# Performance work log

Measured on AMD Instinct MI355X. Metric: run time of the kernel, lower is better.

The kernel has to match this reference:

```python
import jax, jax.numpy as jnp
import numpy as np

N_NODES = 8192
N_EDGES = 49152
IN_F, HID, H1, H2, OUT_F = 128, 64, 64, 5, 32
N_BONDS = 64


def setup_inputs() -> dict:
    key = jax.random.key(0)
    ks = jax.random.split(key, 12)
    s = 0.05
    return {
        "x": jax.random.normal(ks[0], (N_NODES, IN_F), jnp.float32),
        "edge_index": jax.random.randint(ks[1], (2, N_EDGES), 0, N_NODES, jnp.int32),
        "lefts": jax.random.randint(ks[2], (N_BONDS,), 0, N_NODES, jnp.int32),
        "rights": jax.random.randint(ks[3], (N_BONDS,), 0, N_NODES, jnp.int32),
        "W1": jax.random.normal(ks[4], (H1 * HID, IN_F), jnp.float32) * s,
        "att_src1": jax.random.normal(ks[5], (H1, HID), jnp.float32) * s,
        "att_dst1": jax.random.normal(ks[6], (H1, HID), jnp.float32) * s,
        "b1": jnp.zeros((H1 * HID,), jnp.float32),
        "W2": jax.random.normal(ks[7], (H2 * OUT_F, H1 * HID), jnp.float32) * s,
        "att_src2": jax.random.normal(ks[8], (H2, OUT_F), jnp.float32) * s,
        "att_dst2": jax.random.normal(ks[9], (H2, OUT_F), jnp.float32) * s,
        "b2": jnp.zeros((OUT_F,), jnp.float32),
    }


def _gat_conv(x, src, dst, W, a_src, a_dst, b, concat):
    # x: [N, F_in]; W: [H*C, F_in]; a_src/a_dst: [H, C]
    N = x.shape[0]
    H, C = a_src.shape
    h = (x @ W.T).reshape(N, H, C)                    # [N, H, C]
    alpha_s = jnp.einsum("nhc,hc->nh", h, a_src)      # [N, H]
    alpha_d = jnp.einsum("nhc,hc->nh", h, a_dst)
    logits = jax.nn.leaky_relu(alpha_s[src] + alpha_d[dst], negative_slope=0.2)  # [E, H]
    # scatter-softmax over incoming edges of each destination node
    m = jax.ops.segment_max(logits, dst, num_segments=N)
    e = jnp.exp(logits - m[dst])
    denom = jax.ops.segment_sum(e, dst, num_segments=N)
    alpha = e / denom[dst]                            # [E, H]
    msg = h[src] * alpha[:, :, None]                  # [E, H, C]
    out = jax.ops.segment_sum(msg, dst, num_segments=N)  # [N, H, C]
    out = out.reshape(N, H * C) if concat else out.mean(axis=1)
    return out + b


def reference(x, edge_index, lefts, rights, W1, att_src1, att_dst1, b1,
              W2, att_src2, att_dst2, b2):
    N = x.shape[0]
    loops = jnp.arange(N, dtype=edge_index.dtype)
    src = jnp.concatenate([edge_index[0], loops])
    dst = jnp.concatenate([edge_index[1], loops])
    x1 = jax.nn.elu(_gat_conv(x, src, dst, W1, att_src1, att_dst1, b1, concat=True))
    x2 = _gat_conv(x1, src, dst, W2, att_src2, att_dst2, b2, concat=False)  # [N, OUT_F]
    score = (x2[lefts] + x2[rights]).sum(axis=-1)     # [N_BONDS]
    return jax.nn.softmax(score, axis=0)
```

## Files before the change

kernel.cpp:

```cpp
#include <hip/hip_runtime.h>
#include <hip/hip_bf16.h>
#include <math.h>

#define N_NODES  8192
#define N_EDGES  49152
#define E_TOT    57344
#define IN_F     128
#define HID      64
#define NH1      64
#define NH2      5
#define OUT_F    32
#define F1       4096
#define F2       160
#define N_BONDS  64
#define ET       16
#define NP       4
#define HG       16

typedef short bf16x8 __attribute__((ext_vector_type(8)));
typedef float f32x4  __attribute__((ext_vector_type(4)));

__device__ __forceinline__ float lrelu(float x){ return x > 0.f ? x : 0.2f*x; }

__device__ __forceinline__ unsigned short bf16_rne(float f){
    unsigned u = __float_as_uint(f);
    unsigned r = u + 0x7FFF + ((u >> 16) & 1);
    return (unsigned short)(r >> 16);
}
__device__ __forceinline__ float bf16f(unsigned short h){
    return __uint_as_float((unsigned)h << 16);
}

__device__ __forceinline__ void block_sync_lds(){
    asm volatile("s_waitcnt lgkmcnt(0)" ::: "memory");
    __builtin_amdgcn_s_barrier();
    asm volatile("" ::: "memory");
}

__global__ void k_init_counts(int* counts){
    int i = blockIdx.x*256 + threadIdx.x;
    if (i < N_NODES) counts[i] = 1;
}
__global__ void k_count(const int* __restrict__ ei, int* counts){
    int i = blockIdx.x*256 + threadIdx.x;
    if (i < N_EDGES) atomicAdd(&counts[ei[N_EDGES + i]], 1);
}
__global__ __launch_bounds__(1024) void k_scan(const int* __restrict__ counts,
                                               int* __restrict__ row_start,
                                               int* __restrict__ cursor){
    __shared__ int sd[1024];
    int t = threadIdx.x;
    int v[8]; int sum = 0;
    #pragma unroll
    for (int i=0;i<8;i++){ v[i] = counts[t*8+i]; sum += v[i]; }
    sd[t] = sum; __syncthreads();
    for (int off=1; off<1024; off<<=1){
        int vv = (t >= off) ? sd[t-off] : 0;
        __syncthreads();
        sd[t] += vv;
        __syncthreads();
    }
    int run = sd[t] - sum;
    #pragma unroll
    for (int i=0;i<8;i++){ row_start[t*8+i] = run; cursor[t*8+i] = run; run += v[i]; }
    if (t == 1023) row_start[N_NODES] = run;
}
__global__ void k_fill(const int* __restrict__ ei, int* cursor, int* __restrict__ csr_src){
    int i = blockIdx.x*256 + threadIdx.x;
    if (i >= E_TOT) return;
    int s, d;
    if (i < N_EDGES){ s = ei[i]; d = ei[N_EDGES + i]; }
    else { s = i - N_EDGES; d = s; }
    int pos = atomicAdd(&cursor[d], 1);
    csr_src[pos] = s;
}

__global__ void k_packw1d(const float* __restrict__ W1,
                          unsigned short* __restrict__ fh, unsigned short* __restrict__ fl){
    int g = blockIdx.x*256 + threadIdx.x;
    int lane = g & 63, ct = (g >> 6) & 3, ks = (g >> 8) & 3, hg = g >> 10;
    int col = hg*64 + ct*16 + (lane & 15);
    int k = ks*32 + (lane >> 4)*8;
    const float* src = W1 + (size_t)col*IN_F + k;
    bf16x8 hv, lv;
    #pragma unroll
    for (int j=0;j<8;j++){
        float f = src[j];
        unsigned short hb = bf16_rne(f);
        hv[j] = (short)hb;
        lv[j] = (short)bf16_rne(f - bf16f(hb));
    }
    *(bf16x8*)(fh + (size_t)g*8) = hv;
    *(bf16x8*)(fl + (size_t)g*8) = lv;
}

__global__ void k_packw2d(const float* __restrict__ W2,
                          unsigned short* __restrict__ fh, unsigned short* __restrict__ fl){
    int g = blockIdx.x*256 + threadIdx.x;
    int lane = g & 63, ni = (g >> 6) % 10, kc = g / 640;
    int n = ni*16 + (lane & 15);
    int k = kc*32 + (lane >> 4)*8;
    const float* src = W2 + (size_t)n*F1 + k;
    bf16x8 hv, lv;
    #pragma unroll
    for (int j=0;j<8;j++){
        float f = src[j];
        unsigned short hb = bf16_rne(f);
        hv[j] = (short)hb;
        lv[j] = (short)bf16_rne(f - bf16f(hb));
    }
    *(bf16x8*)(fh + (size_t)g*8) = hv;
    *(bf16x8*)(fl + (size_t)g*8) = lv;
}

__global__ __launch_bounds__(128) void k_attvec(const float* __restrict__ W1,
        const float* __restrict__ a_s, const float* __restrict__ a_d,
        float* __restrict__ vsT, float* __restrict__ vdT){
    int h = blockIdx.x, k = threadIdx.x;
    float s = 0.f, d = 0.f;
    for (int c = 0; c < HID; c++){
        float w = W1[(size_t)(h*HID + c)*IN_F + k];
        s += a_s[h*HID + c] * w;
        d += a_d[h*HID + c] * w;
    }
    vsT[k*NH1 + h] = s;
    vdT[k*NH1 + h] = d;
}

__global__ __launch_bounds__(128) void k_alpha1x(const float* __restrict__ x,
        const float* __restrict__ vsT, const float* __restrict__ vdT,
        float* __restrict__ as1, float* __restrict__ ad1){
    int n = blockIdx.x, t = threadIdx.x;
    __shared__ float xs[IN_F];
    xs[t] = x[(size_t)n*IN_F + t];
    __syncthreads();
    if (t < NH1){
        float s = 0.f, d = 0.f;
        for (int k = 0; k < IN_F; k++){
            float xv = xs[k];
            s += xv * vsT[k*NH1 + t];
            d += xv * vdT[k*NH1 + t];
        }
        as1[n*NH1 + t] = s;
        ad1[n*NH1 + t] = d;
    }
}

__global__ __launch_bounds__(256) void k_aggx64(const float* __restrict__ x,
        const float* __restrict__ as1, const float* __restrict__ ad1,
        const int* __restrict__ row_start, const int* __restrict__ csr_src,
        unsigned short* __restrict__ txhi){
    int n = blockIdx.x, t = threadIdx.x;
    __shared__ float ad_s[NH1];
    __shared__ float wt[ET][NH1];
    __shared__ int   st[ET];
    __shared__ float xs[ET][IN_F];
    int e0 = row_start[n], e1 = row_start[n+1];
    if (t < NH1) ad_s[t] = ad1[n*NH1 + t];
    int hq = t >> 4, f0 = (t & 15)*8;
    float acc[4][8] = {};
    float D[4] = {0.f, 0.f, 0.f, 0.f};
    for (int eb = e0; eb < e1; eb += ET){
        int ne = min(ET, e1 - eb);
        if (t < ne) st[t] = csr_src[eb + t];
        __syncthreads();
        for (int idx = t; idx < ne*32; idx += 256){
            int e = idx >> 5, f4 = idx & 31;
            *(float4*)&xs[e][f4*4] = *(const float4*)(x + (size_t)st[e]*IN_F + f4*4);
        }
        for (int idx = t; idx < ne*NH1; idx += 256){
            int e = idx >> 6, hh = idx & 63;
            wt[e][hh] = expf(lrelu(as1[st[e]*NH1 + hh] + ad_s[hh]));
        }
        __syncthreads();
        for (int e = 0; e < ne; e++){
            float4 v0 = *(const float4*)&xs[e][f0];
            float4 v1 = *(const float4*)&xs[e][f0+4];
            float xv[8] = {v0.x,v0.y,v0.z,v0.w,v1.x,v1.y,v1.z,v1.w};
            #pragma unroll
            for (int c=0;c<4;c++){
                float w = wt[e][hq*4 + c];
                D[c] += w;
                #pragma unroll
                for (int j=0;j<8;j++) acc[c][j] += w*xv[j];
            }
        }
        __syncthreads();
    }
    #pragma unroll
    for (int c=0;c<4;c++){
        float dinv = 1.f / D[c];
        bf16x8 hv;
        #pragma unroll
        for (int j=0;j<8;j++) hv[j] = (short)bf16_rne(acc[c][j] * dinv);
        size_t o = ((size_t)(hq*4 + c)*N_NODES + n)*IN_F + f0;
        *(bf16x8*)(txhi + o) = hv;
    }
}

__global__ __launch_bounds__(512, 2) void k_gemm12(
        const unsigned short* __restrict__ txhi,
        const unsigned short* __restrict__ w1fh, const unsigned short* __restrict__ w1fl,
        const unsigned short* __restrict__ w2fh, const unsigned short* __restrict__ w2fl,
        const float* __restrict__ b1,
        float* __restrict__ P){
    __shared__ __attribute__((aligned(16))) unsigned short Als[16384];
    __shared__ __attribute__((aligned(16))) unsigned short W1s[16384];
    __shared__ __attribute__((aligned(16))) unsigned short W2s[20480];
    __shared__ __attribute__((aligned(16))) unsigned short X1s[8192];

    const int tid  = threadIdx.x;
    const int wave = tid >> 6, lane = tid & 63;
    const int wr = wave >> 1, wc = wave & 1;
    const int q = lane >> 4, l16 = lane & 15;
    const int row0 = blockIdx.x * 128;
    const int g = blockIdx.y;
    const int h0 = g * HG;

    bf16x8 pa[4], pw1[4], pw2[5];
    {
        const unsigned short* ab = txhi + ((size_t)h0*N_NODES + row0)*IN_F;
        #pragma unroll
        for (int r=0;r<4;r++) pa[r] = *(const bf16x8*)(ab + r*4096 + tid*8);
        #pragma unroll
        for (int r=0;r<2;r++){
            pw1[r]   = *(const bf16x8*)(w1fh + (size_t)h0*8192 + r*4096 + tid*8);
            pw1[2+r] = *(const bf16x8*)(w1fl + (size_t)h0*8192 + r*4096 + tid*8);
        }
        #pragma unroll
        for (int r=0;r<5;r++){
            int so = r*4096 + tid*8;
            const unsigned short* s = (so < 10240) ? (w2fh + (size_t)h0*10240 + so)
                                                   : (w2fl + (size_t)h0*10240 + (so - 10240));
            pw2[r] = *(const bf16x8*)s;
        }
        #pragma unroll
        for (int r=0;r<4;r++){
            int so = r*4096 + tid*8;
            int sidx = so ^ (((so >> 7) & 7) << 3);
            *(bf16x8*)&Als[sidx] = pa[r];
        }
    }

    f32x4 acc2[2][5] = {};

    #pragma unroll 1
    for (int hh = 0; hh < HG; hh++){
        const int h = h0 + hh;
        block_sync_lds();
        #pragma unroll
        for (int r=0;r<4;r++) *(bf16x8*)&W1s[r*4096 + tid*8] = pw1[r];
        #pragma unroll
        for (int r=0;r<5;r++) *(bf16x8*)&W2s[r*4096 + tid*8] = pw2[r];
        const int hn = (hh+1 < HG) ? (h+1) : h;
        {
            const unsigned short* ab = txhi + ((size_t)hn*N_NODES + row0)*IN_F;
            #pragma unroll
            for (int r=0;r<4;r++) pa[r] = *(const bf16x8*)(ab + r*4096 + tid*8);
            #pragma unroll
            for (int r=0;r<2;r++){
                pw1[r]   = *(const bf16x8*)(w1fh + (size_t)hn*8192 + r*4096 + tid*8);
                pw1[2+r] = *(const bf16x8*)(w1fl + (size_t)hn*8192 + r*4096 + tid*8);
            }
            #pragma unroll
            for (int r=0;r<5;r++){
                int so = r*4096 + tid*8;
                const unsigned short* s = (so < 10240) ? (w2fh + (size_t)hn*10240 + so)
                                                       : (w2fl + (size_t)hn*10240 + (so - 10240));
                pw2[r] = *(const bf16x8*)s;
            }
        }
        block_sync_lds();
        bf16x8 af[2][4];
        #pragma unroll
        for (int mi=0;mi<2;mi++){
            int row = (2*wr+mi)*16 + l16;
            #pragma unroll
            for (int ks=0;ks<4;ks++){
                int sidx = (row*128 + ks*32 + q*8) ^ ((row & 7) << 3);
                af[mi][ks] = *(const bf16x8*)&Als[sidx];
            }
        }
        f32x4 c1[2][2] = {};
        #pragma unroll
        for (int ks=0;ks<4;ks++){
            bf16x8 bh[2], bl[2];
            #pragma unroll
            for (int ni=0;ni<2;ni++){
                int f = (ks*4 + 2*wc + ni)*512 + lane*8;
                bh[ni] = *(const bf16x8*)&W1s[f];
                bl[ni] = *(const bf16x8*)&W1s[8192 + f];
            }
            #pragma unroll
            for (int mi=0;mi<2;mi++)
                #pragma unroll
                for (int ni=0;ni<2;ni++){
                    c1[mi][ni] = __builtin_amdgcn_mfma_f32_16x16x32_bf16(af[mi][ks], bh[ni], c1[mi][ni], 0,0,0);
                    c1[mi][ni] = __builtin_amdgcn_mfma_f32_16x16x32_bf16(af[mi][ks], bl[ni], c1[mi][ni], 0,0,0);
                }
        }
        #pragma unroll
        for (int ni=0;ni<2;ni++){
            int col = (2*wc+ni)*16 + l16;
            float b = b1[h*64 + col];
            #pragma unroll
            for (int mi=0;mi<2;mi++){
                #pragma unroll
                for (int i=0;i<4;i++){
                    float v = c1[mi][ni][i] + b;
                    float o = v > 0.f ? v : expm1f(v);
                    int row = (2*wr+mi)*16 + q*4 + i;
                    int sidx = (row*64 + col) ^ ((row & 7) << 3);
                    X1s[sidx] = bf16_rne(o);
                }
            }
        }
        block_sync_lds();
        bf16x8 a2[2][2];
        #pragma unroll
        for (int mi=0;mi<2;mi++){
            int row = (2*wr+mi)*16 + l16;
            #pragma unroll
            for (int ks=0;ks<2;ks++){
                int sidx = (row*64 + ks*32 + q*8) ^ ((row & 7) << 3);
                a2[mi][ks] = *(const bf16x8*)&X1s[sidx];
            }
        }
        #pragma unroll
        for (int ks=0;ks<2;ks++){
            bf16x8 bh[5], bl[5];
            #pragma unroll
            for (int ni=0;ni<5;ni++){
                int f = (ks*10 + wc*5 + ni)*512 + lane*8;
                bh[ni] = *(const bf16x8*)&W2s[f];
                bl[ni] = *(const bf16x8*)&W2s[10240 + f];
            }
            #pragma unroll
            for (int mi=0;mi<2;mi++)
                #pragma unroll
                for (int ni=0;ni<5;ni++){
                    acc2[mi][ni] = __builtin_amdgcn_mfma_f32_16x16x32_bf16(a2[mi][ks], bh[ni], acc2[mi][ni], 0,0,0);
                    acc2[mi][ni] = __builtin_amdgcn_mfma_f32_16x16x32_bf16(a2[mi][ks], bl[ni], acc2[mi][ni], 0,0,0);
                }
        }
        #pragma unroll
        for (int r=0;r<4;r++){
            int so = r*4096 + tid*8;
            int sidx = so ^ (((so >> 7) & 7) << 3);
            *(bf16x8*)&Als[sidx] = pa[r];
        }
    }

    float* outp = P + ((size_t)g*N_NODES + row0)*F2;
    #pragma unroll
    for (int mi=0;mi<2;mi++)
        #pragma unroll
        for (int ni=0;ni<5;ni++)
            #pragma unroll
            for (int i=0;i<4;i++){
                int rr = (2*wr+mi)*16 + q*4 + i;
                int cc = wc*80 + ni*16 + l16;
                outp[(size_t)rr*F2 + cc] = acc2[mi][ni][i];
            }
}

__global__ __launch_bounds__(256) void k_reduce(const float* __restrict__ P,
                                                float* __restrict__ h2){
    const int NV = N_NODES*F2/4;
    int i = blockIdx.x*256 + threadIdx.x;
    float4 a = ((const float4*)P)[i];
    #pragma unroll
    for (int kb = 1; kb < NP; kb++){
        float4 b = ((const float4*)P)[(size_t)kb*NV + i];
        a.x += b.x; a.y += b.y; a.z += b.z; a.w += b.w;
    }
    ((float4*)h2)[i] = a;
}

__global__ __launch_bounds__(64) void k_alpha2(const float* __restrict__ h2,
        const float* __restrict__ att_s, const float* __restrict__ att_d,
        float* __restrict__ as2, float* __restrict__ ad2){
    int n = blockIdx.x, t = threadIdx.x;
    float ps = 0.f, pd = 0.f;
    if (t < 40){
        float4 h = *(const float4*)(h2 + (size_t)n*F2 + t*4);
        float4 a = ((const float4*)att_s)[t];
        float4 d = ((const float4*)att_d)[t];
        ps = h.x*a.x + h.y*a.y + h.z*a.z + h.w*a.w;
        pd = h.x*d.x + h.y*d.y + h.z*d.z + h.w*d.w;
    }
    ps += __shfl_xor(ps,1); ps += __shfl_xor(ps,2); ps += __shfl_xor(ps,4);
    pd += __shfl_xor(pd,1); pd += __shfl_xor(pd,2); pd += __shfl_xor(pd,4);
    if (t < 40 && (t & 7) == 0){
        as2[n*NH2 + (t>>3)] = ps;
        ad2[n*NH2 + (t>>3)] = pd;
    }
}

__global__ __launch_bounds__(256) void k_agg2(const float* __restrict__ h2,
        const float* __restrict__ as2, const float* __restrict__ ad2,
        const int* __restrict__ row_start, const int* __restrict__ csr_src,
        const float* __restrict__ b2, float* __restrict__ x2){
    int n = blockIdx.x, t = threadIdx.x;
    __shared__ float ad_s[NH2], den_s[NH2], sacc[F2];
    int e0 = row_start[n], e1 = row_start[n+1];
    if (t < NH2) ad_s[t] = ad2[n*NH2 + t];
    __syncthreads();
    if (t < NH2){
        float d = 0.f;
        for (int e=e0;e<e1;e++){
            int s = csr_src[e];
            d += expf(lrelu(as2[s*NH2 + t] + ad_s[t]));
        }
        den_s[t] = d;
    }
    __syncthreads();
    if (t < F2){
        int h = t >> 5;
        float adh  = ad_s[h];
        float dinv = 1.f/den_s[h];
        float acc = 0.f;
        for (int e=e0;e<e1;e++){
            int s = csr_src[e];
            float w = expf(lrelu(as2[s*NH2 + h] + adh)) * dinv;
            acc += w * h2[(size_t)s*F2 + t];
        }
        sacc[t] = acc;
    }
    __syncthreads();
    if (t < OUT_F){
        float v = (sacc[t] + sacc[t+32] + sacc[t+64] + sacc[t+96] + sacc[t+128]) * 0.2f + b2[t];
        x2[n*OUT_F + t] = v;
    }
}

__global__ __launch_bounds__(64) void k_bond(const float* __restrict__ x2,
        const int* __restrict__ lefts, const int* __restrict__ rights,
        float* __restrict__ out){
    int b = threadIdx.x;
    int L = lefts[b], R = rights[b];
    float s = 0.f;
    #pragma unroll
    for (int c=0;c<OUT_F;c+=4){
        float4 l4 = *(const float4*)(x2 + (size_t)L*OUT_F + c);
        float4 r4 = *(const float4*)(x2 + (size_t)R*OUT_F + c);
        s += l4.x+l4.y+l4.z+l4.w + r4.x+r4.y+r4.z+r4.w;
    }
    float m = s;
    #pragma unroll
    for (int off=1; off<64; off<<=1) m = fmaxf(m, __shfl_xor(m, off));
    float e = expf(s - m);
    float sum = e;
    #pragma unroll
    for (int off=1; off<64; off<<=1) sum += __shfl_xor(sum, off);
    out[b] = e / sum;
}

extern "C" void kernel_launch(void* const* d_in, const int* in_sizes, int n_in,
                              void* d_out, int out_size, void* d_ws, size_t ws_size,
                              hipStream_t stream){
    const float* x      = (const float*)d_in[0];
    const int*   ei     = (const int*)  d_in[1];
    const int*   lefts  = (const int*)  d_in[2];
    const int*   rights = (const int*)  d_in[3];
    const float* W1     = (const float*)d_in[4];
    const float* att_s1 = (const float*)d_in[5];
    const float* att_d1 = (const float*)d_in[6];
    const float* b1     = (const float*)d_in[7];
    const float* W2     = (const float*)d_in[8];
    const float* att_s2 = (const float*)d_in[9];
    const float* att_d2 = (const float*)d_in[10];
    const float* b2     = (const float*)d_in[11];
    float* out = (float*)d_out;

    char* ws = (char*)d_ws;
    size_t off = 0;
    auto alloc = [&](size_t bytes) -> void* {
        void* p = ws + off;
        off += (bytes + 255) & ~(size_t)255;
        return p;
    };
    unsigned short* txhi = (unsigned short*)alloc((size_t)NH1*N_NODES*IN_F*2);
    float* part   = (float*)alloc((size_t)NP*N_NODES*F2*4);
    float* h2     = (float*)alloc((size_t)N_NODES*F2*4);
    float* as1    = (float*)alloc((size_t)N_NODES*NH1*4);
    float* ad1    = (float*)alloc((size_t)N_NODES*NH1*4);
    float* as2    = (float*)alloc((size_t)N_NODES*NH2*4);
    float* ad2    = (float*)alloc((size_t)N_NODES*NH2*4);
    float* x2     = (float*)alloc((size_t)N_NODES*OUT_F*4);
    float* vsT    = (float*)alloc((size_t)IN_F*NH1*4);
    float* vdT    = (float*)alloc((size_t)IN_F*NH1*4);
    unsigned short* w1fh = (unsigned short*)alloc((size_t)F1*IN_F*2);
    unsigned short* w1fl = (unsigned short*)alloc((size_t)F1*IN_F*2);
    unsigned short* w2fh = (unsigned short*)alloc((size_t)128*10*512*2);
    unsigned short* w2fl = (unsigned short*)alloc((size_t)128*10*512*2);
    int* counts    = (int*)alloc((size_t)N_NODES*4);
    int* row_start = (int*)alloc((size_t)(N_NODES+1)*4);
    int* cursor    = (int*)alloc((size_t)N_NODES*4);
    int* csr_src   = (int*)alloc((size_t)E_TOT*4);

    k_init_counts<<<32, 256, 0, stream>>>(counts);
    k_count<<<192, 256, 0, stream>>>(ei, counts);
    k_scan<<<1, 1024, 0, stream>>>(counts, row_start, cursor);
    k_fill<<<224, 256, 0, stream>>>(ei, cursor, csr_src);

    k_packw1d<<<65536/256, 256, 0, stream>>>(W1, w1fh, w1fl);
    k_packw2d<<<81920/256, 256, 0, stream>>>(W2, w2fh, w2fl);

    k_attvec<<<NH1, 128, 0, stream>>>(W1, att_s1, att_d1, vsT, vdT);
    k_alpha1x<<<N_NODES, 128, 0, stream>>>(x, vsT, vdT, as1, ad1);

    k_aggx64<<<N_NODES, 256, 0, stream>>>(x, as1, ad1, row_start, csr_src, txhi);

    k_gemm12<<<dim3(64, NP), 512, 0, stream>>>(txhi, w1fh, w1fl, w2fh, w2fl, b1, part);
    k_reduce<<<N_NODES*F2/4/256, 256, 0, stream>>>(part, h2);

    k_alpha2<<<N_NODES, 64, 0, stream>>>(h2, att_s2, att_d2, as2, ad2);
    k_agg2<<<N_NODES, 256, 0, stream>>>(h2, as2, ad2, row_start, csr_src, b2, x2);

    k_bond<<<1, 64, 0, stream>>>(x2, lefts, rights, out);
}
```

Baseline: 260.8 us.

## Read GEMM A operand directly from global, halve LDS, raise occupancy

Drops the LDS staging buffer for the A tile and loads the A fragments straight from global memory inside the k-loop. The W2 low-half weights are read directly from global instead of through LDS, which halves W2s. Less LDS and fewer registers let the launch bounds ask for 4 blocks per CU. The head group is split into 8 partitions of 8 heads each instead of 4 of 16, giving more blocks. The cost is uncoalesced, row-strided global loads in the inner loop with no prefetch to hide their latency, plus more partial results for the reduction kernel to sum.

```diff
diff --git a/kernel.cpp b/kernel.cpp
--- a/kernel.cpp
+++ b/kernel.cpp
@@ -14,10 +14,11 @@
 #define F2       160
 #define N_BONDS  64
 #define ET       16
-#define NP       4
-#define HG       16
+#define NP       8
+#define HG       8
 
 typedef short bf16x8 __attribute__((ext_vector_type(8)));
+typedef short bf16x4 __attribute__((ext_vector_type(4)));
 typedef float f32x4  __attribute__((ext_vector_type(4)));
 
 __device__ __forceinline__ float lrelu(float x){ return x > 0.f ? x : 0.2f*x; }
@@ -198,15 +199,14 @@
     }
 }
 
-__global__ __launch_bounds__(512, 2) void k_gemm12(
+__global__ __launch_bounds__(512, 4) void k_gemm12(
         const unsigned short* __restrict__ txhi,
         const unsigned short* __restrict__ w1fh, const unsigned short* __restrict__ w1fl,
         const unsigned short* __restrict__ w2fh, const unsigned short* __restrict__ w2fl,
         const float* __restrict__ b1,
         float* __restrict__ P){
-    __shared__ __attribute__((aligned(16))) unsigned short Als[16384];
     __shared__ __attribute__((aligned(16))) unsigned short W1s[16384];
-    __shared__ __attribute__((aligned(16))) unsigned short W2s[20480];
+    __shared__ __attribute__((aligned(16))) unsigned short W2s[10240];
     __shared__ __attribute__((aligned(16))) unsigned short X1s[8192];
 
     const int tid  = threadIdx.x;
@@ -217,29 +217,15 @@
     const int g = blockIdx.y;
     const int h0 = g * HG;
 
-    bf16x8 pa[4], pw1[4], pw2[5];
+    bf16x8 pw1[4], pw2[2]; bf16x4 pw2t;
     {
-        const unsigned short* ab = txhi + ((size_t)h0*N_NODES + row0)*IN_F;
-        #pragma unroll
-        for (int r=0;r<4;r++) pa[r] = *(const bf16x8*)(ab + r*4096 + tid*8);
         #pragma unroll
         for (int r=0;r<2;r++){
             pw1[r]   = *(const bf16x8*)(w1fh + (size_t)h0*8192 + r*4096 + tid*8);
             pw1[2+r] = *(const bf16x8*)(w1fl + (size_t)h0*8192 + r*4096 + tid*8);
-        }
-        #pragma unroll
-        for (int r=0;r<5;r++){
-            int so = r*4096 + tid*8;
-            const unsigned short* s = (so < 10240) ? (w2fh + (size_t)h0*10240 + so)
-                                                   : (w2fl + (size_t)h0*10240 + (so - 10240));
-            pw2[r] = *(const bf16x8*)s;
-        }
-        #pragma unroll
-        for (int r=0;r<4;r++){
-            int so = r*4096 + tid*8;
-            int sidx = so ^ (((so >> 7) & 7) << 3);
-            *(bf16x8*)&Als[sidx] = pa[r];
-        }
+            pw2[r]   = *(const bf16x8*)(w2fh + (size_t)h0*10240 + r*4096 + tid*8);
+        }
+        pw2t = *(const bf16x4*)(w2fh + (size_t)h0*10240 + 8192 + tid*4);
     }
 
     f32x4 acc2[2][5] = {};
@@ -251,39 +237,29 @@
         #pragma unroll
         for (int r=0;r<4;r++) *(bf16x8*)&W1s[r*4096 + tid*8] = pw1[r];
         #pragma unroll
-        for (int r=0;r<5;r++) *(bf16x8*)&W2s[r*4096 + tid*8] = pw2[r];
+        for (int r=0;r<2;r++) *(bf16x8*)&W2s[r*4096 + tid*8] = pw2[r];
+        *(bf16x4*)&W2s[8192 + tid*4] = pw2t;
         const int hn = (hh+1 < HG) ? (h+1) : h;
         {
-            const unsigned short* ab = txhi + ((size_t)hn*N_NODES + row0)*IN_F;
-            #pragma unroll
-            for (int r=0;r<4;r++) pa[r] = *(const bf16x8*)(ab + r*4096 + tid*8);
             #pragma unroll
             for (int r=0;r<2;r++){
                 pw1[r]   = *(const bf16x8*)(w1fh + (size_t)hn*8192 + r*4096 + tid*8);
                 pw1[2+r] = *(const bf16x8*)(w1fl + (size_t)hn*8192 + r*4096 + tid*8);
-            }
-            #pragma unroll
-            for (int r=0;r<5;r++){
-                int so = r*4096 + tid*8;
-                const unsigned short* s = (so < 10240) ? (w2fh + (size_t)hn*10240 + so)
-                                                       : (w2fl + (size_t)hn*10240 + (so - 10240));
-                pw2[r] = *(const bf16x8*)s;
-            }
+                pw2[r]   = *(const bf16x8*)(w2fh + (size_t)hn*10240 + r*4096 + tid*8);
+            }
+            pw2t = *(const bf16x4*)(w2fh + (size_t)hn*10240 + 8192 + tid*4);
         }
         block_sync_lds();
-        bf16x8 af[2][4];
-        #pragma unroll
-        for (int mi=0;mi<2;mi++){
-            int row = (2*wr+mi)*16 + l16;
-            #pragma unroll
-            for (int ks=0;ks<4;ks++){
-                int sidx = (row*128 + ks*32 + q*8) ^ ((row & 7) << 3);
-                af[mi][ks] = *(const bf16x8*)&Als[sidx];
-            }
-        }
+        const unsigned short* Abase = txhi + ((size_t)h*N_NODES + row0)*IN_F;
         f32x4 c1[2][2] = {};
         #pragma unroll
         for (int ks=0;ks<4;ks++){
+            bf16x8 af[2];
+            #pragma unroll
+            for (int mi=0;mi<2;mi++){
+                int row = (2*wr+mi)*16 + l16;
+                af[mi] = *(const bf16x8*)(Abase + (size_t)row*IN_F + ks*32 + q*8);
+            }
             bf16x8 bh[2], bl[2];
             #pragma unroll
             for (int ni=0;ni<2;ni++){
@@ -295,8 +271,8 @@
             for (int mi=0;mi<2;mi++)
                 #pragma unroll
                 for (int ni=0;ni<2;ni++){
-                    c1[mi][ni] = __builtin_amdgcn_mfma_f32_16x16x32_bf16(af[mi][ks], bh[ni], c1[mi][ni], 0,0,0);
-                    c1[mi][ni] = __builtin_amdgcn_mfma_f32_16x16x32_bf16(af[mi][ks], bl[ni], c1[mi][ni], 0,0,0);
+                    c1[mi][ni] = __builtin_amdgcn_mfma_f32_16x16x32_bf16(af[mi], bh[ni], c1[mi][ni], 0,0,0);
+                    c1[mi][ni] = __builtin_amdgcn_mfma_f32_16x16x32_bf16(af[mi], bl[ni], c1[mi][ni], 0,0,0);
                 }
         }
         #pragma unroll
@@ -316,38 +292,29 @@
             }
         }
         block_sync_lds();
-        bf16x8 a2[2][2];
-        #pragma unroll
-        for (int mi=0;mi<2;mi++){
-            int row = (2*wr+mi)*16 + l16;
-            #pragma unroll
-            for (int ks=0;ks<2;ks++){
+        #pragma unroll
+        for (int ks=0;ks<2;ks++){
+            bf16x8 a2[2];
+            #pragma unroll
+            for (int mi=0;mi<2;mi++){
+                int row = (2*wr+mi)*16 + l16;
                 int sidx = (row*64 + ks*32 + q*8) ^ ((row & 7) << 3);
-                a2[mi][ks] = *(const bf16x8*)&X1s[sidx];
-            }
-        }
-        #pragma unroll
-        for (int ks=0;ks<2;ks++){
+                a2[mi] = *(const bf16x8*)&X1s[sidx];
+            }
             bf16x8 bh[5], bl[5];
             #pragma unroll
             for (int ni=0;ni<5;ni++){
                 int f = (ks*10 + wc*5 + ni)*512 + lane*8;
                 bh[ni] = *(const bf16x8*)&W2s[f];
-                bl[ni] = *(const bf16x8*)&W2s[10240 + f];
+                bl[ni] = *(const bf16x8*)(w2fl + (size_t)((h*2 + ks)*10 + wc*5 + ni)*512 + lane*8);
             }
             #pragma unroll
             for (int mi=0;mi<2;mi++)
                 #pragma unroll
                 for (int ni=0;ni<5;ni++){
-                    acc2[mi][ni] = __builtin_amdgcn_mfma_f32_16x16x32_bf16(a2[mi][ks], bh[ni], acc2[mi][ni], 0,0,0);
-                    acc2[mi][ni] = __builtin_amdgcn_mfma_f32_16x16x32_bf16(a2[mi][ks], bl[ni], acc2[mi][ni], 0,0,0);
+                    acc2[mi][ni] = __builtin_amdgcn_mfma_f32_16x16x32_bf16(a2[mi], bh[ni], acc2[mi][ni], 0,0,0);
+                    acc2[mi][ni] = __builtin_amdgcn_mfma_f32_16x16x32_bf16(a2[mi], bl[ni], acc2[mi][ni], 0,0,0);
                 }
-        }
-        #pragma unroll
-        for (int r=0;r<4;r++){
-            int so = r*4096 + tid*8;
-            int sidx = so ^ (((so >> 7) & 7) << 3);
-            *(bf16x8*)&Als[sidx] = pa[r];
         }
     }
 
```

Result: slower. 326.8 us (+25.3%).
